# Performance work log

Measured on AMD Instinct MI355X. Metric: run time of the kernel, lower is better.

Reference implementation:

```python
import jax, jax.numpy as jnp
import numpy as np

NUM_USER = 100000
NUM_ITEM = 50000
N = NUM_USER + NUM_ITEM
EMBED_DIM = 64
LAYERS = 3
NNZ = 5000000
BATCH = 4096


def setup_inputs() -> dict:
    key = jax.random.key(0)
    k_vals, k_u, k_i, k_row, k_col, k_us, k_is = jax.random.split(key, 7)
    vals = jax.random.uniform(k_vals, (NNZ,), dtype=jnp.float32)
    user_table = jax.random.normal(k_u, (NUM_USER, EMBED_DIM), dtype=jnp.float32)
    item_table = jax.random.normal(k_i, (NUM_ITEM, EMBED_DIM), dtype=jnp.float32)
    row = jax.random.randint(k_row, (NNZ,), 0, N, dtype=jnp.int32)
    col = jax.random.randint(k_col, (NNZ,), 0, N, dtype=jnp.int32)
    users = jax.random.randint(k_us, (BATCH,), 0, NUM_USER, dtype=jnp.int32)
    items = jax.random.randint(k_is, (BATCH,), 0, NUM_ITEM, dtype=jnp.int32)
    return {"vals": vals, "user_table": user_table, "item_table": item_table,
            "row": row, "col": col, "users": users, "items": items}


def _spmm(vals, row, col, x):
    # y[r] = sum over edges e with row[e]==r of vals[e] * x[col[e]]  -> [N, d]
    return jax.ops.segment_sum(vals[:, None] * x[col], row, num_segments=N)


def reference(vals, user_table, item_table, row, col, users, items):
    # LightGCN.propagate: multi-hop SpMM + mean over hop embeddings
    embed = jnp.concatenate([user_table, item_table], axis=0)  # [N, d]
    acc = embed
    e = embed
    for _ in range(LAYERS):
        e = _spmm(vals, row, col, e)
        acc = acc + e
    out = acc / jnp.asarray(LAYERS + 1, dtype=acc.dtype)  # mean over layers+1 hops
    user_emb = out[:NUM_USER][users]   # [B, d]
    item_emb = out[NUM_USER:][items]   # [B, d]
    scores = jnp.sum(user_emb * item_emb, axis=1)  # [B]
    return scores
```

## Files before the change

kernel.cpp:

```cpp
#include <hip/hip_runtime.h>

#define NUM_USER 100000
#define NUM_ITEM 50000
#define NNODE 150000
#define EMBED_DIM 64
#define NNZ_CNT 5000000
#define BATCH 4096

#define BROWS 256
#define NBUCK ((NNODE + BROWS - 1) / BROWS)
#define NBLK 512
#define CHUNK ((NNZ_CNT + NBLK - 1) / NBLK)
#define COLMASK 0x3FFFF
#define RLSHIFT 18
#define VSHIFT 18
#define VSCALE (1.0f / 16384.0f)

__device__ __forceinline__ unsigned short f2bf(float f) {
    unsigned b = __float_as_uint(f);
    return (unsigned short)((b + 0x7FFFu + ((b >> 16) & 1u)) >> 16);
}
__device__ __forceinline__ float bf2f(unsigned short u) {
    return __uint_as_float((unsigned)u << 16);
}


__global__ __launch_bounds__(1024) void bhist_local(const int* __restrict__ row,
                                                    int* __restrict__ histT) {
    __shared__ int lh[NBUCK];
    for (int i = threadIdx.x; i < NBUCK; i += blockDim.x) lh[i] = 0;
    __syncthreads();
    const int lo = blockIdx.x * CHUNK;
    const int hi = min(lo + CHUNK, NNZ_CNT);
    for (int e = lo + (int)threadIdx.x; e < hi; e += blockDim.x)
        atomicAdd(&lh[row[e] >> 8], 1);
    __syncthreads();
    for (int i = threadIdx.x; i < NBUCK; i += blockDim.x)
        histT[i * NBLK + blockIdx.x] = lh[i];
}

__global__ __launch_bounds__(512) void scanA(int* __restrict__ histT,
                                             int* __restrict__ btot) {
    const int g = (int)((blockIdx.x * blockDim.x + threadIdx.x) >> 6);
    const int lane = threadIdx.x & 63;
    if (g >= NBUCK) return;
    const int base = g * NBLK + lane * 8;
    int v[8];
    int s = 0;
    #pragma unroll
    for (int u = 0; u < 8; ++u) { v[u] = histT[base + u]; s += v[u]; }
    int pre = s;
    #pragma unroll
    for (int off = 1; off < 64; off <<= 1) {
        int t = __shfl_up(pre, off, 64);
        if (lane >= off) pre += t;
    }
    int excl = pre - s;
    #pragma unroll
    for (int u = 0; u < 8; ++u) { const int w = v[u]; histT[base + u] = excl; excl += w; }
    if (lane == 63) btot[g] = pre;
}

__global__ __launch_bounds__(1024) void scanB(const int* __restrict__ btot,
                                              int* __restrict__ bptr) {
    __shared__ int sums[1024];
    const int t = threadIdx.x;
    const int s = (t < NBUCK) ? btot[t] : 0;
    sums[t] = s;
    __syncthreads();
    for (int off = 1; off < 1024; off <<= 1) {
        int v = (t >= off) ? sums[t - off] : 0;
        __syncthreads();
        sums[t] += v;
        __syncthreads();
    }
    if (t < NBUCK) bptr[t] = sums[t] - s;
    if (t == 0) bptr[NBUCK] = NNZ_CNT;
}

__global__ __launch_bounds__(1024) void bscatter2(const float* __restrict__ vals,
                                                  const int* __restrict__ row,
                                                  const int* __restrict__ col,
                                                  const int* __restrict__ histT,
                                                  const int* __restrict__ bptr,
                                                  int2* __restrict__ grouped) {
    __shared__ int lh[NBUCK];
    const int b = blockIdx.x;
    for (int i = threadIdx.x; i < NBUCK; i += blockDim.x)
        lh[i] = bptr[i] + histT[i * NBLK + b];
    __syncthreads();
    const int lo = b * CHUNK;
    const int hi = min(lo + CHUNK, NNZ_CNT);
    for (int e = lo + (int)threadIdx.x; e < hi; e += blockDim.x) {
        const int r = row[e];
        const int bk = r >> 8;
        const int rl = r & 255;
        const int pos = atomicAdd(&lh[bk], 1);
        grouped[pos] = make_int2(col[e] | (rl << RLSHIFT), __float_as_int(vals[e]));
    }
}

__global__ __launch_bounds__(512) void bucket_sort(const int* __restrict__ bptr,
                                                   const int2* __restrict__ grouped,
                                                   unsigned* __restrict__ csr,
                                                   int* __restrict__ row_ptr) {
    __shared__ int lh[BROWS];
    __shared__ int lbase[BROWS];
    const int b = blockIdx.x;
    const int bstart = bptr[b];
    const int bend   = bptr[b + 1];
    if (threadIdx.x < BROWS) lh[threadIdx.x] = 0;
    __syncthreads();
    for (int e = bstart + (int)threadIdx.x; e < bend; e += blockDim.x)
        atomicAdd(&lh[((unsigned)grouped[e].x) >> RLSHIFT], 1);
    __syncthreads();
    if (threadIdx.x == 0) {
        int run = 0;
        for (int i = 0; i < BROWS; ++i) { const int c = lh[i]; lbase[i] = run; run += c; }
    }
    __syncthreads();
    const int node = b * BROWS + (int)threadIdx.x;
    if (threadIdx.x < BROWS && node < NNODE) row_ptr[node] = bstart + lbase[threadIdx.x];
    if (threadIdx.x < BROWS) lh[threadIdx.x] = lbase[threadIdx.x];
    __syncthreads();
    for (int e = bstart + (int)threadIdx.x; e < bend; e += blockDim.x) {
        const int2 rec = grouped[e];
        const int rl = ((unsigned)rec.x) >> RLSHIFT;
        const int pos = bstart + atomicAdd(&lh[rl], 1);
        unsigned u = (unsigned)(__int_as_float(rec.y) * 16384.0f + 0.5f);
        if (u > 16383u) u = 16383u;
        csr[pos] = (u << VSHIFT) | ((unsigned)rec.x & COLMASK);
    }
}

__global__ void fix_tail(int* __restrict__ row_ptr) {
    row_ptr[NNODE] = NNZ_CNT;
}


__global__ void to_bf16(const float4* __restrict__ ut, const float4* __restrict__ it,
                        ushort4* __restrict__ xbf) {
    const int nu4 = NUM_USER * EMBED_DIM / 4;
    const int nt4 = NNODE * EMBED_DIM / 4;
    int i = blockIdx.x * blockDim.x + threadIdx.x;
    const int stride = gridDim.x * blockDim.x;
    for (; i < nt4; i += stride) {
        const float4 v = (i < nu4) ? ut[i] : it[i - nu4];
        ushort4 o;
        o.x = f2bf(v.x); o.y = f2bf(v.y); o.z = f2bf(v.z); o.w = f2bf(v.w);
        xbf[i] = o;
    }
}


__global__ __launch_bounds__(256) void spmm_pull(const int* __restrict__ row_ptr,
                          const unsigned* __restrict__ csr,
                          const unsigned short* __restrict__ x,
                          unsigned short* __restrict__ y) {
    const int wave = (int)((blockIdx.x * blockDim.x + threadIdx.x) >> 6);
    const int lane = threadIdx.x & 63;
    if (wave >= NNODE) return;
    const int start = __builtin_amdgcn_readfirstlane(row_ptr[wave]);
    const int end   = __builtin_amdgcn_readfirstlane(row_ptr[wave + 1]);
    float acc = 0.f;
    int j = start;
    for (; j + 16 <= end; j += 16) {
        unsigned ee[16]; float xv[16];
        #pragma unroll
        for (int u = 0; u < 16; ++u) {
            __builtin_memcpy(&ee[u], &csr[j + u], 4);
            xv[u] = bf2f(x[(size_t)(ee[u] & COLMASK) * EMBED_DIM + lane]);
        }
        #pragma unroll
        for (int u = 0; u < 16; ++u) acc += (float)(ee[u] >> VSHIFT) * xv[u];
    }
    const int rem = end - j;
    if (rem > 8) {
        float vv[16], xv[16];
        #pragma unroll
        for (int u = 0; u < 16; ++u) {
            const int jj = j + u;
            const int idx = (jj < end) ? jj : end - 1;
            unsigned e; __builtin_memcpy(&e, &csr[idx], 4);
            vv[u] = (jj < end) ? (float)(e >> VSHIFT) : 0.f;
            xv[u] = bf2f(x[(size_t)(e & COLMASK) * EMBED_DIM + lane]);
        }
        #pragma unroll
        for (int u = 0; u < 16; ++u) acc += vv[u] * xv[u];
    } else if (rem > 0) {
        float vv[8], xv[8];
        #pragma unroll
        for (int u = 0; u < 8; ++u) {
            const int jj = j + u;
            const int idx = (jj < end) ? jj : end - 1;
            unsigned e; __builtin_memcpy(&e, &csr[idx], 4);
            vv[u] = (jj < end) ? (float)(e >> VSHIFT) : 0.f;
            xv[u] = bf2f(x[(size_t)(e & COLMASK) * EMBED_DIM + lane]);
        }
        #pragma unroll
        for (int u = 0; u < 8; ++u) acc += vv[u] * xv[u];
    }
    y[(size_t)wave * EMBED_DIM + lane] = f2bf(acc * VSCALE);
}

__global__ __launch_bounds__(256) void batch_pull(const int* __restrict__ row_ptr,
                           const unsigned* __restrict__ csr,
                           const unsigned short* __restrict__ x,
                           const int* __restrict__ users,
                           const int* __restrict__ items,
                           float* __restrict__ uacc,
                           float* __restrict__ iacc) {
    const int g = (int)((blockIdx.x * blockDim.x + threadIdx.x) >> 6);
    const int lane = threadIdx.x & 63;
    if (g >= 2 * BATCH) return;
    const bool is_item = g >= BATCH;
    const int b = is_item ? g - BATCH : g;
    const int node = is_item ? items[b] + NUM_USER : users[b];
    const int start = __builtin_amdgcn_readfirstlane(row_ptr[node]);
    const int end   = __builtin_amdgcn_readfirstlane(row_ptr[node + 1]);
    float acc = 0.f;
    int j = start;
    for (; j + 16 <= end; j += 16) {
        unsigned ee[16]; float xv[16];
        #pragma unroll
        for (int u = 0; u < 16; ++u) {
            __builtin_memcpy(&ee[u], &csr[j + u], 4);
            xv[u] = bf2f(x[(size_t)(ee[u] & COLMASK) * EMBED_DIM + lane]);
        }
        #pragma unroll
        for (int u = 0; u < 16; ++u) acc += (float)(ee[u] >> VSHIFT) * xv[u];
    }
    const int rem = end - j;
    if (rem > 8) {
        float vv[16], xv[16];
        #pragma unroll
        for (int u = 0; u < 16; ++u) {
            const int jj = j + u;
            const int idx = (jj < end) ? jj : end - 1;
            unsigned e; __builtin_memcpy(&e, &csr[idx], 4);
            vv[u] = (jj < end) ? (float)(e >> VSHIFT) : 0.f;
            xv[u] = bf2f(x[(size_t)(e & COLMASK) * EMBED_DIM + lane]);
        }
        #pragma unroll
        for (int u = 0; u < 16; ++u) acc += vv[u] * xv[u];
    } else if (rem > 0) {
        float vv[8], xv[8];
        #pragma unroll
        for (int u = 0; u < 8; ++u) {
            const int jj = j + u;
            const int idx = (jj < end) ? jj : end - 1;
            unsigned e; __builtin_memcpy(&e, &csr[idx], 4);
            vv[u] = (jj < end) ? (float)(e >> VSHIFT) : 0.f;
            xv[u] = bf2f(x[(size_t)(e & COLMASK) * EMBED_DIM + lane]);
        }
        #pragma unroll
        for (int u = 0; u < 8; ++u) acc += vv[u] * xv[u];
    }
    float* dst = is_item ? iacc : uacc;
    dst[(size_t)b * EMBED_DIM + lane] += acc * VSCALE;
}


__global__ void init_acc(const float* __restrict__ user_table,
                         const float* __restrict__ item_table,
                         const int* __restrict__ users,
                         const int* __restrict__ items,
                         float* __restrict__ uacc,
                         float* __restrict__ iacc) {
    const int tid = blockIdx.x * blockDim.x + threadIdx.x;
    const int b = tid >> 6;
    const int k = tid & 63;
    uacc[tid] = user_table[(size_t)users[b] * EMBED_DIM + k];
    iacc[tid] = item_table[(size_t)items[b] * EMBED_DIM + k];
}

__global__ void gather_add(const unsigned short* __restrict__ src,
                           const int* __restrict__ users,
                           const int* __restrict__ items,
                           float* __restrict__ uacc,
                           float* __restrict__ iacc) {
    const int tid = blockIdx.x * blockDim.x + threadIdx.x;
    const int b = tid >> 6;
    const int k = tid & 63;
    uacc[tid] += bf2f(src[(size_t)users[b] * EMBED_DIM + k]);
    iacc[tid] += bf2f(src[((size_t)items[b] + NUM_USER) * EMBED_DIM + k]);
}

__global__ void score_kernel(const float* __restrict__ uacc,
                             const float* __restrict__ iacc,
                             float* __restrict__ out) {
    const int tid = blockIdx.x * blockDim.x + threadIdx.x;
    const int b = tid >> 6;
    const int k = tid & 63;
    float p = uacc[tid] * iacc[tid];
    #pragma unroll
    for (int off = 32; off > 0; off >>= 1) p += __shfl_down(p, off, 64);
    if (k == 0) out[b] = p * (1.0f / 16.0f);
}


extern "C" void kernel_launch(void* const* d_in, const int* in_sizes, int n_in,
                              void* d_out, int out_size, void* d_ws, size_t ws_size,
                              hipStream_t stream) {
    const float* vals       = (const float*)d_in[0];
    const float* user_table = (const float*)d_in[1];
    const float* item_table = (const float*)d_in[2];
    const int*   row        = (const int*)d_in[3];
    const int*   col        = (const int*)d_in[4];
    const int*   users      = (const int*)d_in[5];
    const int*   items      = (const int*)d_in[6];
    float* out = (float*)d_out;

    char* ws = (char*)d_ws;
    size_t off = 0;
    auto alloc = [&](size_t bytes) { char* p = ws + off; off += (bytes + 255) & ~(size_t)255; return p; };
    const size_t NBH = (size_t)NNODE * EMBED_DIM * sizeof(unsigned short);
    unsigned short* xbf  = (unsigned short*)alloc(NBH);
    unsigned short* bufA = (unsigned short*)alloc(NBH);
    int2*  grouped = (int2*)alloc((size_t)NNZ_CNT * sizeof(int2));
    unsigned* csr  = (unsigned*)alloc((size_t)NNZ_CNT * sizeof(unsigned));
    int*   row_ptr = (int*)alloc((size_t)(NNODE + 1) * sizeof(int));
    int*   bptr    = (int*)alloc((size_t)(NBUCK + 1) * sizeof(int));
    int*   btot    = (int*)alloc((size_t)NBUCK * sizeof(int));
    int*   histT   = (int*)alloc((size_t)NBUCK * NBLK * sizeof(int));
    float* uacc    = (float*)alloc((size_t)BATCH * EMBED_DIM * sizeof(float));
    float* iacc    = (float*)alloc((size_t)BATCH * EMBED_DIM * sizeof(float));

    bhist_local<<<NBLK, 1024, 0, stream>>>(row, histT);
    scanA<<<(NBUCK * 64 + 511) / 512, 512, 0, stream>>>(histT, btot);
    scanB<<<1, 1024, 0, stream>>>(btot, bptr);
    bscatter2<<<NBLK, 1024, 0, stream>>>(vals, row, col, histT, bptr, grouped);
    bucket_sort<<<NBUCK, 512, 0, stream>>>(bptr, grouped, csr, row_ptr);
    fix_tail<<<1, 1, 0, stream>>>(row_ptr);

    to_bf16<<<2048, 256, 0, stream>>>((const float4*)user_table,
                                      (const float4*)item_table, (ushort4*)xbf);

    init_acc<<<(BATCH * EMBED_DIM) / 256, 256, 0, stream>>>(user_table, item_table,
                                                            users, items, uacc, iacc);
    spmm_pull<<<(NNODE + 3) / 4, 256, 0, stream>>>(row_ptr, csr, xbf, bufA);
    gather_add<<<(BATCH * EMBED_DIM) / 256, 256, 0, stream>>>(bufA, users, items, uacc, iacc);
    unsigned short* bufB = (unsigned short*)grouped;
    spmm_pull<<<(NNODE + 3) / 4, 256, 0, stream>>>(row_ptr, csr, bufA, bufB);
    gather_add<<<(BATCH * EMBED_DIM) / 256, 256, 0, stream>>>(bufB, users, items, uacc, iacc);
    batch_pull<<<(2 * BATCH * 64) / 256, 256, 0, stream>>>(row_ptr, csr, bufB,
                                                           users, items, uacc, iacc);
    score_kernel<<<(BATCH * EMBED_DIM) / 256, 256, 0, stream>>>(uacc, iacc, out);
}
```

Baseline: 297.9 us.

## Vectorize COO preprocessing loads and split SpMM wave into two half-row gathers

The histogram and scatter kernels now read row/col/vals as int4/float4 vectors, using a chunk size that is a multiple of 4, and the bucket sort unrolls its passes four ways to raise memory-level parallelism. The SpMM pull kernel now has each half-wave handle alternate edges, with every lane loading two packed bf16 values as one 32-bit word. The two halves are combined with a cross-half shuffle and written back as packed pairs. This halves the number of gather instructions per edge and doubles the edges in flight, at the cost of a shuffle reduction and a lane-0..31-only store.

```diff
diff --git a/kernel.cpp b/kernel.cpp
--- a/kernel.cpp
+++ b/kernel.cpp
@@ -10,7 +10,7 @@
 #define BROWS 256
 #define NBUCK ((NNODE + BROWS - 1) / BROWS)
 #define NBLK 512
-#define CHUNK ((NNZ_CNT + NBLK - 1) / NBLK)
+#define CHUNK4 9768
 #define COLMASK 0x3FFFF
 #define RLSHIFT 18
 #define VSHIFT 18
@@ -30,10 +30,20 @@
     __shared__ int lh[NBUCK];
     for (int i = threadIdx.x; i < NBUCK; i += blockDim.x) lh[i] = 0;
     __syncthreads();
-    const int lo = blockIdx.x * CHUNK;
-    const int hi = min(lo + CHUNK, NNZ_CNT);
-    for (int e = lo + (int)threadIdx.x; e < hi; e += blockDim.x)
-        atomicAdd(&lh[row[e] >> 8], 1);
+    const int lo = blockIdx.x * CHUNK4;
+    const int hi = min(lo + CHUNK4, NNZ_CNT);
+    for (int base = lo; base < hi; base += 4096) {
+        const int e0 = base + (int)threadIdx.x * 4;
+        if (e0 + 4 <= hi) {
+            const int4 r4 = *(const int4*)&row[e0];
+            atomicAdd(&lh[r4.x >> 8], 1);
+            atomicAdd(&lh[r4.y >> 8], 1);
+            atomicAdd(&lh[r4.z >> 8], 1);
+            atomicAdd(&lh[r4.w >> 8], 1);
+        } else if (e0 < hi) {
+            for (int e = e0; e < hi; ++e) atomicAdd(&lh[row[e] >> 8], 1);
+        }
+    }
     __syncthreads();
     for (int i = threadIdx.x; i < NBUCK; i += blockDim.x)
         histT[i * NBLK + blockIdx.x] = lh[i];
@@ -89,14 +99,29 @@
     for (int i = threadIdx.x; i < NBUCK; i += blockDim.x)
         lh[i] = bptr[i] + histT[i * NBLK + b];
     __syncthreads();
-    const int lo = b * CHUNK;
-    const int hi = min(lo + CHUNK, NNZ_CNT);
-    for (int e = lo + (int)threadIdx.x; e < hi; e += blockDim.x) {
-        const int r = row[e];
-        const int bk = r >> 8;
-        const int rl = r & 255;
-        const int pos = atomicAdd(&lh[bk], 1);
-        grouped[pos] = make_int2(col[e] | (rl << RLSHIFT), __float_as_int(vals[e]));
+    const int lo = b * CHUNK4;
+    const int hi = min(lo + CHUNK4, NNZ_CNT);
+    for (int base = lo; base < hi; base += 4096) {
+        const int e0 = base + (int)threadIdx.x * 4;
+        if (e0 + 4 <= hi) {
+            const int4   r4 = *(const int4*)&row[e0];
+            const int4   c4 = *(const int4*)&col[e0];
+            const float4 v4 = *(const float4*)&vals[e0];
+            const int p0 = atomicAdd(&lh[r4.x >> 8], 1);
+            const int p1 = atomicAdd(&lh[r4.y >> 8], 1);
+            const int p2 = atomicAdd(&lh[r4.z >> 8], 1);
+            const int p3 = atomicAdd(&lh[r4.w >> 8], 1);
+            grouped[p0] = make_int2(c4.x | ((r4.x & 255) << RLSHIFT), __float_as_int(v4.x));
+            grouped[p1] = make_int2(c4.y | ((r4.y & 255) << RLSHIFT), __float_as_int(v4.y));
+            grouped[p2] = make_int2(c4.z | ((r4.z & 255) << RLSHIFT), __float_as_int(v4.z));
+            grouped[p3] = make_int2(c4.w | ((r4.w & 255) << RLSHIFT), __float_as_int(v4.w));
+        } else if (e0 < hi) {
+            for (int e = e0; e < hi; ++e) {
+                const int r = row[e];
+                const int pos = atomicAdd(&lh[r >> 8], 1);
+                grouped[pos] = make_int2(col[e] | ((r & 255) << RLSHIFT), __float_as_int(vals[e]));
+            }
+        }
     }
 }
 
@@ -111,7 +136,18 @@
     const int bend   = bptr[b + 1];
     if (threadIdx.x < BROWS) lh[threadIdx.x] = 0;
     __syncthreads();
-    for (int e = bstart + (int)threadIdx.x; e < bend; e += blockDim.x)
+    int e = bstart + (int)threadIdx.x;
+    for (; e + 1536 < bend; e += 2048) {
+        const unsigned x0 = (unsigned)grouped[e].x;
+        const unsigned x1 = (unsigned)grouped[e + 512].x;
+        const unsigned x2 = (unsigned)grouped[e + 1024].x;
+        const unsigned x3 = (unsigned)grouped[e + 1536].x;
+        atomicAdd(&lh[x0 >> RLSHIFT], 1);
+        atomicAdd(&lh[x1 >> RLSHIFT], 1);
+        atomicAdd(&lh[x2 >> RLSHIFT], 1);
+        atomicAdd(&lh[x3 >> RLSHIFT], 1);
+    }
+    for (; e < bend; e += 512)
         atomicAdd(&lh[((unsigned)grouped[e].x) >> RLSHIFT], 1);
     __syncthreads();
     if (threadIdx.x == 0) {
@@ -123,14 +159,22 @@
     if (threadIdx.x < BROWS && node < NNODE) row_ptr[node] = bstart + lbase[threadIdx.x];
     if (threadIdx.x < BROWS) lh[threadIdx.x] = lbase[threadIdx.x];
     __syncthreads();
-    for (int e = bstart + (int)threadIdx.x; e < bend; e += blockDim.x) {
-        const int2 rec = grouped[e];
+    auto emit = [&](int2 rec) {
         const int rl = ((unsigned)rec.x) >> RLSHIFT;
         const int pos = bstart + atomicAdd(&lh[rl], 1);
         unsigned u = (unsigned)(__int_as_float(rec.y) * 16384.0f + 0.5f);
         if (u > 16383u) u = 16383u;
         csr[pos] = (u << VSHIFT) | ((unsigned)rec.x & COLMASK);
-    }
+    };
+    e = bstart + (int)threadIdx.x;
+    for (; e + 1536 < bend; e += 2048) {
+        const int2 r0 = grouped[e];
+        const int2 r1 = grouped[e + 512];
+        const int2 r2 = grouped[e + 1024];
+        const int2 r3 = grouped[e + 1536];
+        emit(r0); emit(r1); emit(r2); emit(r3);
+    }
+    for (; e < bend; e += 512) emit(grouped[e]);
 }
 
 __global__ void fix_tail(int* __restrict__ row_ptr) {
@@ -160,47 +204,63 @@
     const int wave = (int)((blockIdx.x * blockDim.x + threadIdx.x) >> 6);
     const int lane = threadIdx.x & 63;
     if (wave >= NNODE) return;
+    const int half = lane >> 5;
+    const int c2   = lane & 31;
     const int start = __builtin_amdgcn_readfirstlane(row_ptr[wave]);
     const int end   = __builtin_amdgcn_readfirstlane(row_ptr[wave + 1]);
-    float acc = 0.f;
+    float ax = 0.f, ay = 0.f;
     int j = start;
     for (; j + 16 <= end; j += 16) {
-        unsigned ee[16]; float xv[16];
-        #pragma unroll
-        for (int u = 0; u < 16; ++u) {
-            __builtin_memcpy(&ee[u], &csr[j + u], 4);
-            xv[u] = bf2f(x[(size_t)(ee[u] & COLMASK) * EMBED_DIM + lane]);
-        }
-        #pragma unroll
-        for (int u = 0; u < 16; ++u) acc += (float)(ee[u] >> VSHIFT) * xv[u];
+        unsigned ee[16];
+        #pragma unroll
+        for (int u = 0; u < 16; ++u) __builtin_memcpy(&ee[u], &csr[j + u], 4);
+        unsigned w[8]; float vv[8];
+        #pragma unroll
+        for (int p = 0; p < 8; ++p) {
+            const unsigned e = half ? ee[2 * p + 1] : ee[2 * p];
+            w[p] = *(const unsigned*)((const char*)x +
+                     (size_t)(e & COLMASK) * 128 + (size_t)c2 * 4);
+            vv[p] = (float)(e >> VSHIFT);
+        }
+        #pragma unroll
+        for (int p = 0; p < 8; ++p) {
+            ax += vv[p] * __uint_as_float(w[p] << 16);
+            ay += vv[p] * __uint_as_float(w[p] & 0xFFFF0000u);
+        }
     }
     const int rem = end - j;
     if (rem > 8) {
-        float vv[16], xv[16];
-        #pragma unroll
-        for (int u = 0; u < 16; ++u) {
-            const int jj = j + u;
-            const int idx = (jj < end) ? jj : end - 1;
+        #pragma unroll
+        for (int p = 0; p < 8; ++p) {
+            const int j0 = j + 2 * p + half;
+            const int idx = (j0 < end) ? j0 : end - 1;
             unsigned e; __builtin_memcpy(&e, &csr[idx], 4);
-            vv[u] = (jj < end) ? (float)(e >> VSHIFT) : 0.f;
-            xv[u] = bf2f(x[(size_t)(e & COLMASK) * EMBED_DIM + lane]);
-        }
-        #pragma unroll
-        for (int u = 0; u < 16; ++u) acc += vv[u] * xv[u];
+            const float v = (j0 < end) ? (float)(e >> VSHIFT) : 0.f;
+            const unsigned w0 = *(const unsigned*)((const char*)x +
+                     (size_t)(e & COLMASK) * 128 + (size_t)c2 * 4);
+            ax += v * __uint_as_float(w0 << 16);
+            ay += v * __uint_as_float(w0 & 0xFFFF0000u);
+        }
     } else if (rem > 0) {
-        float vv[8], xv[8];
-        #pragma unroll
-        for (int u = 0; u < 8; ++u) {
-            const int jj = j + u;
-            const int idx = (jj < end) ? jj : end - 1;
+        #pragma unroll
+        for (int p = 0; p < 4; ++p) {
+            const int j0 = j + 2 * p + half;
+            const int idx = (j0 < end) ? j0 : end - 1;
             unsigned e; __builtin_memcpy(&e, &csr[idx], 4);
-            vv[u] = (jj < end) ? (float)(e >> VSHIFT) : 0.f;
-            xv[u] = bf2f(x[(size_t)(e & COLMASK) * EMBED_DIM + lane]);
-        }
-        #pragma unroll
-        for (int u = 0; u < 8; ++u) acc += vv[u] * xv[u];
-    }
-    y[(size_t)wave * EMBED_DIM + lane] = f2bf(acc * VSCALE);
+            const float v = (j0 < end) ? (float)(e >> VSHIFT) : 0.f;
+            const unsigned w0 = *(const unsigned*)((const char*)x +
+                     (size_t)(e & COLMASK) * 128 + (size_t)c2 * 4);
+            ax += v * __uint_as_float(w0 << 16);
+            ay += v * __uint_as_float(w0 & 0xFFFF0000u);
+        }
+    }
+    ax += __shfl_xor(ax, 32, 64);
+    ay += __shfl_xor(ay, 32, 64);
+    if (half == 0) {
+        const unsigned lo = f2bf(ax * VSCALE);
+        const unsigned hi = f2bf(ay * VSCALE);
+        ((unsigned*)y)[(size_t)wave * 32 + c2] = (hi << 16) | lo;
+    }
 }
 
 __global__ __launch_bounds__(256) void batch_pull(const int* __restrict__ row_ptr,
```

Result: slower. 499.7 us (+67.7%).
